# Optimization experiments

Measured on AMD Instinct MI355X. Metric: run time of the kernel, lower is better.

## Reference

```python
import jax, jax.numpy as jnp
import numpy as np

N_TIME = 512          # n_time_nodes
LATENT = 32           # latent_dim
HIDDEN = 64           # hidden_dim
N_MODES = 8           # r_fourier_modes
X_A0 = 0.3            # initial stoichiometry (anode)
CSANMAX = 28700.0     # max concentration scale
BASE_LOGIT = float(np.log(X_A0 / (1.0 - X_A0)))  # logit_from_fraction(x_a0)
FEAT_DIM = 1 + 2 * N_MODES   # [rho, cos(k*pi*rho), sin(k*pi*rho)]
IN_DIM = LATENT + FEAT_DIM
N_POINTS = 2_000_000


def setup_inputs() -> dict:
    key = jax.random.key(0)
    ks = jax.random.split(key, 8)
    time_idx = jax.random.randint(ks[0], (N_POINTS,), 0, N_TIME)
    rho = jax.random.uniform(ks[1], (N_POINTS,), dtype=jnp.float32)
    # trainable latent code per nonzero time node
    emb = jax.random.normal(ks[2], (N_TIME - 1, LATENT), dtype=jnp.float32) * 0.02
    # decoder_a: Linear(IN,HID)+SiLU, Linear(HID,HID)+SiLU, Linear(HID,1)
    W0 = jax.random.normal(ks[3], (IN_DIM, HIDDEN), dtype=jnp.float32) / np.sqrt(IN_DIM)
    b0 = jnp.zeros((HIDDEN,), jnp.float32)
    W1 = jax.random.normal(ks[4], (HIDDEN, HIDDEN), dtype=jnp.float32) / np.sqrt(HIDDEN)
    b1 = jnp.zeros((HIDDEN,), jnp.float32)
    Wout = jax.random.normal(ks[5], (HIDDEN, 1), dtype=jnp.float32) * 0.1
    bout = jnp.zeros((1,), jnp.float32)
    return {"time_idx": time_idx, "rho": rho, "emb": emb,
            "W0": W0, "b0": b0, "W1": W1, "b1": b1, "Wout": Wout, "bout": bout}


def _radius_features(rho):
    # [N] -> [N, 1 + 2*N_MODES]
    k = jnp.arange(1, N_MODES + 1, dtype=rho.dtype)
    ang = jnp.pi * rho[:, None] * k[None, :]
    return jnp.concatenate([rho[:, None], jnp.cos(ang), jnp.sin(ang)], axis=1)


def reference(time_idx, rho, emb, W0, b0, W1, b1, Wout, bout):
    # predicated version of the torch masked scatter: compute everywhere,
    # select initial-condition value where time_idx == 0
    idx = jnp.clip(time_idx - 1, 0, N_TIME - 2)       # safe gather index
    e = emb[idx]                                       # [N, LATENT]
    feat = _radius_features(rho)                       # [N, FEAT_DIM]
    h = jnp.concatenate([e, feat], axis=1)             # [N, IN_DIM]
    h = jax.nn.silu(h @ W0 + b0)
    h = jax.nn.silu(h @ W1 + b1)
    raw = (h @ Wout + bout)[:, 0]                      # [N]
    theta = jax.nn.sigmoid(raw + BASE_LOGIT)
    return jnp.where(time_idx == 0, X_A0 * CSANMAX, theta * CSANMAX)
```

## Files before the change

kernel.cpp:

```cpp
#include <hip/hip_runtime.h>
#include <stdint.h>


typedef _Float16 half8  __attribute__((ext_vector_type(8)));
typedef _Float16 half4v __attribute__((ext_vector_type(4)));
typedef _Float16 half2v __attribute__((ext_vector_type(2)));
typedef float f32x4 __attribute__((ext_vector_type(4)));

#define LOG2E 1.44269504088896340736f
#define BASE_LOGIT -0.84729786038720367f
#define CSANMAX 28700.0f
#define IC_VAL 8610.0f

__device__ __forceinline__ float fast_exp2(float x) { return __builtin_amdgcn_exp2f(x); }
__device__ __forceinline__ float fast_rcp(float x)  { return __builtin_amdgcn_rcpf(x); }
__device__ __forceinline__ float sigf(float x)  { return fast_rcp(1.0f + fast_exp2(-LOG2E * x)); }
__device__ __forceinline__ float siluf(float x) { return x * sigf(x); }
__device__ __forceinline__ half2v pkh(float a, float b) {
  return __builtin_bit_cast(half2v, __builtin_amdgcn_cvt_pkrtz(a, b));
}

union H8 { half8 v8; half2v v2[4]; };
union H4 { half4v v4; half2v v2[2]; };

template <int CTRL>
__device__ __forceinline__ float dpp_radd(float x) {
  int yi = __builtin_amdgcn_update_dpp(0, __builtin_bit_cast(int, x), CTRL, 0xF, 0xF, false);
  return x + __builtin_bit_cast(float, yi);
}
__device__ __forceinline__ float row_sum16(float x) {
  x = dpp_radd<0xB1>(x);
  x = dpp_radd<0x4E>(x);
  x = dpp_radd<0x141>(x);
  x = dpp_radd<0x140>(x);
  return x;
}

__global__ __launch_bounds__(128) void mlp_kernel(
    const int* __restrict__ tix, const float* __restrict__ rho,
    const float* __restrict__ emb, const float* __restrict__ W0,
    const float* __restrict__ b0, const float* __restrict__ W1,
    const float* __restrict__ b1, const float* __restrict__ Wout,
    const float* __restrict__ bout, float* __restrict__ out, int ngroups)
{
  __shared__ __align__(16) _Float16 ldsF[2][64][40];
  __shared__ __align__(16) _Float16 ldsH[2][2][16][72];

  const int tid  = threadIdx.x;
  const int wid  = tid >> 6;
  const int lane = tid & 63;
  const int m    = lane & 15;
  const int q    = lane >> 4;

  _Float16 (*F)[40]      = ldsF[wid];
  _Float16 (*Hd)[16][72] = ldsH[wid];

  half8 B0f[4][2], B1f[4][2];
#pragma unroll
  for (int t = 0; t < 4; ++t) {
#pragma unroll
    for (int s = 0; s < 2; ++s) {
      half8 f0, f1;
#pragma unroll
      for (int j = 0; j < 8; ++j) {
        const int k = s * 32 + q * 8 + j;
        const int n = t * 16 + m;
        const float v0 = (k < 49) ? W0[k * 64 + n] : ((k == 49) ? b0[n] : 0.0f);
        f0[j] = (_Float16)v0;
        f1[j] = (_Float16)W1[k * 64 + n];
      }
      B0f[t][s] = f0;
      B1f[t][s] = f1;
    }
  }
  float b1n[4], woutm[4];
#pragma unroll
  for (int t = 0; t < 4; ++t) {
    b1n[t]   = b1[t * 16 + m];
    woutm[t] = Wout[t * 16 + m];
  }
  const float boutBL = bout[0] + BASE_LOGIT;

  {
    half8 zc = (half8)(_Float16)0.0f;
    *(half8*)&F[lane][16] = zc;
    *(half8*)&F[lane][24] = zc;
  }

  const f32x4 z = {0.0f, 0.0f, 0.0f, 0.0f};
  const int gwaves = gridDim.x * 2;

  for (int g = blockIdx.x * 2 + wid; g < ngroups; g += gwaves) {
    const int gbase = g * 64;

    const int   tiL = tix[gbase + lane];
    const float rh  = rho[gbase + lane];
    const float rev = 0.5f * rh;
    const float c1 = __builtin_amdgcn_cosf(rev);
    const float s1 = __builtin_amdgcn_sinf(rev);
    float cs[8], sn[8];
    cs[0] = c1; sn[0] = s1;
    {
      float cm2 = 1.0f, cm1 = c1, sm2 = 0.0f, sm1 = s1;
      const float tc = 2.0f * c1;
#pragma unroll
      for (int k = 1; k < 8; ++k) {
        const float ck = tc * cm1 - cm2;
        const float sk = tc * sm1 - sm2;
        cs[k] = ck; sn[k] = sk;
        cm2 = cm1; cm1 = ck; sm2 = sm1; sm1 = sk;
      }
    }
    H8 h0, h1;
    h0.v2[0] = pkh(rh,    cs[0]); h0.v2[1] = pkh(cs[1], cs[2]);
    h0.v2[2] = pkh(cs[3], cs[4]); h0.v2[3] = pkh(cs[5], cs[6]);
    h1.v2[0] = pkh(cs[7], sn[0]); h1.v2[1] = pkh(sn[1], sn[2]);
    h1.v2[2] = pkh(sn[3], sn[4]); h1.v2[3] = pkh(sn[5], sn[6]);
    *(half8*)&F[lane][0] = h0.v8;
    *(half8*)&F[lane][8] = h1.v8;
    *(half2v*)&F[lane][16] = pkh(sn[7], 1.0f);

    float dcar = 0.0f;

#pragma unroll
    for (int st = 0; st < 4; ++st) {
      _Float16 (*Hb)[72] = Hd[st & 1];

      const int tim  = __shfl(tiL, st * 16 + m, 64);
      const int idxm = min(max(tim - 1, 0), 510);
      const float* erow = emb + (size_t)idxm * 32 + q * 8;
      const f32x4 e0 = *(const f32x4*)erow;
      const f32x4 e1 = *(const f32x4*)(erow + 4);
      H8 X0;
      X0.v2[0] = pkh(e0[0], e0[1]); X0.v2[1] = pkh(e0[2], e0[3]);
      X0.v2[2] = pkh(e1[0], e1[1]); X0.v2[3] = pkh(e1[2], e1[3]);
      const half8 X1 = *(const half8*)&F[st * 16 + m][q * 8];

      f32x4 acc[4];
#pragma unroll
      for (int t = 0; t < 4; ++t) {
        f32x4 a = __builtin_amdgcn_mfma_f32_16x16x32_f16(B0f[t][0], X0.v8, z, 0, 0, 0);
        a = __builtin_amdgcn_mfma_f32_16x16x32_f16(B0f[t][1], X1, a, 0, 0, 0);
        acc[t] = a;
      }
#pragma unroll
      for (int t = 0; t < 4; ++t) {
        H4 hh;
        hh.v2[0] = pkh(siluf(acc[t][0]), siluf(acc[t][1]));
        hh.v2[1] = pkh(siluf(acc[t][2]), siluf(acc[t][3]));
        *(half4v*)&Hb[m][t * 16 + q * 4] = hh.v4;
      }

      const half8 Y0 = *(const half8*)&Hb[m][q * 8];
      const half8 Y1 = *(const half8*)&Hb[m][32 + q * 8];
#pragma unroll
      for (int t = 0; t < 4; ++t) {
        const f32x4 binit = {b1n[t], b1n[t], b1n[t], b1n[t]};
        f32x4 a = __builtin_amdgcn_mfma_f32_16x16x32_f16(Y0, B1f[t][0], binit, 0, 0, 0);
        a = __builtin_amdgcn_mfma_f32_16x16x32_f16(Y1, B1f[t][1], a, 0, 0, 0);
        acc[t] = a;
      }
      float dot0 = 0.0f, dot1 = 0.0f, dot2 = 0.0f, dot3 = 0.0f;
#pragma unroll
      for (int t = 0; t < 4; ++t) {
        dot0 = fmaf(siluf(acc[t][0]), woutm[t], dot0);
        dot1 = fmaf(siluf(acc[t][1]), woutm[t], dot1);
        dot2 = fmaf(siluf(acc[t][2]), woutm[t], dot2);
        dot3 = fmaf(siluf(acc[t][3]), woutm[t], dot3);
      }
      dot0 = row_sum16(dot0);
      dot1 = row_sum16(dot1);
      dot2 = row_sum16(dot2);
      dot3 = row_sum16(dot3);
      const float dsel = (m & 2) ? ((m & 1) ? dot3 : dot2) : ((m & 1) ? dot1 : dot0);
      const float dg = __shfl(dsel, (m >> 2) * 16 + (m & 3), 64);
      dcar = (q == st) ? dg : dcar;
    }

    const float theta = sigf(dcar + boutBL);
    out[gbase + lane] = (tiL == 0) ? IC_VAL : theta * CSANMAX;
  }
}

extern "C" void kernel_launch(void* const* d_in, const int* in_sizes, int n_in,
                              void* d_out, int out_size, void* d_ws, size_t ws_size,
                              hipStream_t stream) {
  const int*   tix  = (const int*)d_in[0];
  const float* rho  = (const float*)d_in[1];
  const float* emb  = (const float*)d_in[2];
  const float* W0   = (const float*)d_in[3];
  const float* b0   = (const float*)d_in[4];
  const float* W1   = (const float*)d_in[5];
  const float* b1   = (const float*)d_in[6];
  const float* Wout = (const float*)d_in[7];
  const float* bout = (const float*)d_in[8];
  float* outp = (float*)d_out;

  const int n       = in_sizes[0];
  const int ngroups = n / 64;

  int grid = 2048;
  if (grid * 2 > ngroups) grid = (ngroups + 1) / 2;
  mlp_kernel<<<dim3(grid), dim3(128), 0, stream>>>(
      tix, rho, emb, W0, b0, W1, b1, Wout, bout, outp, ngroups);
}
```

Before: 174.7 us.

## Prefetch next group inputs and embedding rows; pair SiLU reciprocals

Software-pipelines the grid-stride loop. The next group's time indices and rho are loaded one iteration ahead, and within each group the embedding row for the next 16-row step is loaded before the current step's MFMAs, hiding global and gather latency. SiLU is also computed in pairs that share one reciprocal (rcp of the product of the two denominators), halving rcp instructions at the cost of extra multiplies and a small overflow risk when both exponentials are large. The change adds register pressure from the in-flight prefetched values.

```diff
diff --git a/kernel.cpp b/kernel.cpp
--- a/kernel.cpp
+++ b/kernel.cpp
@@ -15,7 +15,13 @@
 __device__ __forceinline__ float fast_exp2(float x) { return __builtin_amdgcn_exp2f(x); }
 __device__ __forceinline__ float fast_rcp(float x)  { return __builtin_amdgcn_rcpf(x); }
 __device__ __forceinline__ float sigf(float x)  { return fast_rcp(1.0f + fast_exp2(-LOG2E * x)); }
-__device__ __forceinline__ float siluf(float x) { return x * sigf(x); }
+__device__ __forceinline__ void silu2(float x0, float x1, float& y0, float& y1) {
+  const float d0 = 1.0f + fast_exp2(-LOG2E * x0);
+  const float d1 = 1.0f + fast_exp2(-LOG2E * x1);
+  const float r  = fast_rcp(d0 * d1);
+  y0 = x0 * d1 * r;
+  y1 = x1 * d0 * r;
+}
 __device__ __forceinline__ half2v pkh(float a, float b) {
   return __builtin_bit_cast(half2v, __builtin_amdgcn_cvt_pkrtz(a, b));
 }
@@ -90,11 +96,26 @@
   const f32x4 z = {0.0f, 0.0f, 0.0f, 0.0f};
   const int gwaves = gridDim.x * 2;
 
-  for (int g = blockIdx.x * 2 + wid; g < ngroups; g += gwaves) {
+  int g = blockIdx.x * 2 + wid;
+  if (g >= ngroups) return;
+
+  int   tiL = tix[g * 64 + lane];
+  float rh  = rho[g * 64 + lane];
+
+  for (; g < ngroups; g += gwaves) {
     const int gbase = g * 64;
 
-    const int   tiL = tix[gbase + lane];
-    const float rh  = rho[gbase + lane];
+    const int gn = (g + gwaves < ngroups) ? (g + gwaves) : g;
+    const int   tiLn = tix[gn * 64 + lane];
+    const float rhn  = rho[gn * 64 + lane];
+
+    int tim4[4];
+#pragma unroll
+    for (int st = 0; st < 4; ++st) tim4[st] = __shfl(tiL, st * 16 + m, 64);
+    const float* erow0 = emb + (size_t)min(max(tim4[0] - 1, 0), 510) * 32 + q * 8;
+    f32x4 eA0 = *(const f32x4*)erow0;
+    f32x4 eA1 = *(const f32x4*)(erow0 + 4);
+
     const float rev = 0.5f * rh;
     const float c1 = __builtin_amdgcn_cosf(rev);
     const float s1 = __builtin_amdgcn_sinf(rev);
@@ -126,14 +147,16 @@
     for (int st = 0; st < 4; ++st) {
       _Float16 (*Hb)[72] = Hd[st & 1];
 
-      const int tim  = __shfl(tiL, st * 16 + m, 64);
-      const int idxm = min(max(tim - 1, 0), 510);
-      const float* erow = emb + (size_t)idxm * 32 + q * 8;
-      const f32x4 e0 = *(const f32x4*)erow;
-      const f32x4 e1 = *(const f32x4*)(erow + 4);
+      f32x4 eB0, eB1;
+      if (st < 3) {
+        const float* erown = emb + (size_t)min(max(tim4[st + 1] - 1, 0), 510) * 32 + q * 8;
+        eB0 = *(const f32x4*)erown;
+        eB1 = *(const f32x4*)(erown + 4);
+      }
+
       H8 X0;
-      X0.v2[0] = pkh(e0[0], e0[1]); X0.v2[1] = pkh(e0[2], e0[3]);
-      X0.v2[2] = pkh(e1[0], e1[1]); X0.v2[3] = pkh(e1[2], e1[3]);
+      X0.v2[0] = pkh(eA0[0], eA0[1]); X0.v2[1] = pkh(eA0[2], eA0[3]);
+      X0.v2[2] = pkh(eA1[0], eA1[1]); X0.v2[3] = pkh(eA1[2], eA1[3]);
       const half8 X1 = *(const half8*)&F[st * 16 + m][q * 8];
 
       f32x4 acc[4];
@@ -145,9 +168,12 @@
       }
 #pragma unroll
       for (int t = 0; t < 4; ++t) {
+        float s0, s1v, s2, s3;
+        silu2(acc[t][0], acc[t][1], s0, s1v);
+        silu2(acc[t][2], acc[t][3], s2, s3);
         H4 hh;
-        hh.v2[0] = pkh(siluf(acc[t][0]), siluf(acc[t][1]));
-        hh.v2[1] = pkh(siluf(acc[t][2]), siluf(acc[t][3]));
+        hh.v2[0] = pkh(s0, s1v);
+        hh.v2[1] = pkh(s2, s3);
         *(half4v*)&Hb[m][t * 16 + q * 4] = hh.v4;
       }
 
@@ -163,10 +189,13 @@
       float dot0 = 0.0f, dot1 = 0.0f, dot2 = 0.0f, dot3 = 0.0f;
 #pragma unroll
       for (int t = 0; t < 4; ++t) {
-        dot0 = fmaf(siluf(acc[t][0]), woutm[t], dot0);
-        dot1 = fmaf(siluf(acc[t][1]), woutm[t], dot1);
-        dot2 = fmaf(siluf(acc[t][2]), woutm[t], dot2);
-        dot3 = fmaf(siluf(acc[t][3]), woutm[t], dot3);
+        float s0, s1v, s2, s3;
+        silu2(acc[t][0], acc[t][1], s0, s1v);
+        silu2(acc[t][2], acc[t][3], s2, s3);
+        dot0 = fmaf(s0,  woutm[t], dot0);
+        dot1 = fmaf(s1v, woutm[t], dot1);
+        dot2 = fmaf(s2,  woutm[t], dot2);
+        dot3 = fmaf(s3,  woutm[t], dot3);
       }
       dot0 = row_sum16(dot0);
       dot1 = row_sum16(dot1);
@@ -175,10 +204,14 @@
       const float dsel = (m & 2) ? ((m & 1) ? dot3 : dot2) : ((m & 1) ? dot1 : dot0);
       const float dg = __shfl(dsel, (m >> 2) * 16 + (m & 3), 64);
       dcar = (q == st) ? dg : dcar;
+
+      eA0 = eB0; eA1 = eB1;
     }
 
     const float theta = sigf(dcar + boutBL);
     out[gbase + lane] = (tiL == 0) ? IC_VAL : theta * CSANMAX;
+
+    tiL = tiLn; rh = rhn;
   }
 }
 
```

Result: slower. 178.9 us (+2.4%).
